# Performance work log

Measured on AMD Instinct MI355X. Metric: run time of the kernel, lower is better.

Reference implementation:

```python
import jax, jax.numpy as jnp
import numpy as np

T, B, D, H, L = 1024, 64, 512, 512, 2


def setup_inputs() -> dict:
    key = jax.random.key(0)
    ks = jax.random.split(key, 10)
    s = 1.0 / np.sqrt(D)
    return {
        "x": jax.random.normal(ks[0], (T, B, D), jnp.float32),
        "hidden": jax.random.normal(ks[1], (L, B, H), jnp.float32),
        "fc_w": jax.random.normal(ks[2], (D, D), jnp.float32) * s,
        "fc_b": jax.random.normal(ks[3], (D,), jnp.float32) * s,
        "w0": jax.random.normal(ks[4], (H, D), jnp.float32) * s,
        "b0": jax.random.normal(ks[5], (H,), jnp.float32) * s,
        "u0": jax.random.uniform(ks[6], (H,), jnp.float32, -1.0, 1.0),
        "w1": jax.random.normal(ks[7], (H, H), jnp.float32) * s,
        "b1": jax.random.normal(ks[8], (H,), jnp.float32) * s,
        "u1": jax.random.uniform(ks[9], (H,), jnp.float32, -1.0, 1.0),
    }


def _indrnn_layer(inp, h0, w, b, u):
    # Precompute input projection for all timesteps: [T, B, H]
    pre = jnp.einsum("tbd,hd->tbh", inp, w) + b

    def step(h, p):
        h_new = jax.nn.relu(p + u * h)  # elementwise recurrent weight
        return h_new, h_new

    h_last, outs = jax.lax.scan(step, h0, pre)
    return outs, h_last


def reference(x, hidden, fc_w, fc_b, w0, b0, u0, w1, b1, u1):
    # fc layer before the IndRNN stack
    x = jnp.einsum("tbd,ed->tbe", x, fc_w) + fc_b
    out0, h0 = _indrnn_layer(x, hidden[0], w0, b0, u0)
    out1, h1 = _indrnn_layer(out0, hidden[1], w1, b1, u1)
    hn = jnp.stack([h0, h1], axis=0)  # [L, B, H]
    return out1, hn
```

## Files before the change

kernel.cpp:

```cpp
#include <hip/hip_runtime.h>
#include <hip/hip_bf16.h>
#include <cstdint>
#include <cstddef>

#define T_DIM 1024
#define B_DIM 64
#define D_DIM 512
#define H_DIM 512
#define TBROWS (T_DIM * B_DIM)
#define BH (B_DIM * H_DIM)
#define TBH ((size_t)T_DIM * (size_t)BH)

typedef __bf16 bf16x8 __attribute__((ext_vector_type(8)));
typedef float floatx4 __attribute__((ext_vector_type(4)));

__device__ __forceinline__ void async_load16(const void* g, void* l) {
  __builtin_amdgcn_global_load_lds(
      (const __attribute__((address_space(1))) unsigned int*)g,
      (__attribute__((address_space(3))) unsigned int*)l,
      16, 0, 0);
}

__global__ __launch_bounds__(256) void cvt_bf16_kernel(
    const float* __restrict__ in, __bf16* __restrict__ out, long n) {
  long i = ((long)blockIdx.x * 256 + threadIdx.x) * 8;
  if (i + 8 <= n) {
    const float4 a = *(const float4*)(in + i);
    const float4 b = *(const float4*)(in + i + 4);
    bf16x8 v;
    v[0] = (__bf16)a.x; v[1] = (__bf16)a.y; v[2] = (__bf16)a.z; v[3] = (__bf16)a.w;
    v[4] = (__bf16)b.x; v[5] = (__bf16)b.y; v[6] = (__bf16)b.z; v[7] = (__bf16)b.w;
    *(bf16x8*)(out + i) = v;
  }
}

__global__ __launch_bounds__(256) void fuse_w_kernel(
    const float* __restrict__ w0, const float* __restrict__ fc_w,
    __bf16* __restrict__ W) {
  const int h = blockIdx.x >> 1;
  const int d = ((blockIdx.x & 1) << 8) + threadIdx.x;
  float a0 = 0.f, a1 = 0.f, a2 = 0.f, a3 = 0.f;
  for (int e = 0; e < D_DIM; e += 4) {
    a0 = fmaf(w0[h * D_DIM + e + 0], fc_w[(size_t)(e + 0) * D_DIM + d], a0);
    a1 = fmaf(w0[h * D_DIM + e + 1], fc_w[(size_t)(e + 1) * D_DIM + d], a1);
    a2 = fmaf(w0[h * D_DIM + e + 2], fc_w[(size_t)(e + 2) * D_DIM + d], a2);
    a3 = fmaf(w0[h * D_DIM + e + 3], fc_w[(size_t)(e + 3) * D_DIM + d], a3);
  }
  W[(size_t)h * D_DIM + d] = (__bf16)((a0 + a1) + (a2 + a3));
}

__global__ __launch_bounds__(256) void bcomb_kernel(
    const float* __restrict__ w0, const float* __restrict__ fc_b,
    const float* __restrict__ b0, float* __restrict__ bc) {
  const int h = blockIdx.x * 256 + threadIdx.x;
  float acc = b0[h];
  for (int e = 0; e < D_DIM; ++e)
    acc = fmaf(w0[(size_t)h * D_DIM + e], fc_b[e], acc);
  bc[h] = acc;
}

#define BM 128
#define BN 128
#define BK 32

__global__ __launch_bounds__(256) void gemm_bt_bias(
    const __bf16* __restrict__ A,
    const __bf16* __restrict__ Bm,
    const float* __restrict__ bias,
    float* __restrict__ C,
    int M, int N, int K) {
  __shared__ __bf16 As[BM * BK];
  __shared__ __bf16 Bs[BN * BK];

  const int tid = threadIdx.x;
  const int lane = tid & 63;
  const int wave = tid >> 6;
  const int nb = N / BN;
  const int bm = blockIdx.x / nb;
  const int bn = blockIdx.x % nb;
  const int m0 = bm * BM, n0 = bn * BN;

  floatx4 zero = {0.f, 0.f, 0.f, 0.f};
  floatx4 acc[4][4];
#pragma unroll
  for (int i = 0; i < 4; i++)
#pragma unroll
    for (int j = 0; j < 4; j++) acc[i][j] = zero;

  const int e0 = (wave * 2 + 0) * 64 + lane;
  const int e1 = (wave * 2 + 1) * 64 + lane;
  const int r0 = e0 >> 2, c0 = (e0 & 3) * 8;
  const int r1 = e1 >> 2, c1 = (e1 & 3) * 8;

  const int tm = (wave >> 1) * 64;
  const int tn = (wave & 1) * 64;
  const int lrow = lane & 15;
  const int lk = (lane >> 4) * 8;

  for (int k0 = 0; k0 < K; k0 += BK) {
    async_load16(&A[(size_t)(m0 + r0) * K + k0 + c0], &As[(wave * 2 + 0) * 512]);
    async_load16(&A[(size_t)(m0 + r1) * K + k0 + c1], &As[(wave * 2 + 1) * 512]);
    async_load16(&Bm[(size_t)(n0 + r0) * K + k0 + c0], &Bs[(wave * 2 + 0) * 512]);
    async_load16(&Bm[(size_t)(n0 + r1) * K + k0 + c1], &Bs[(wave * 2 + 1) * 512]);
    __syncthreads();

    bf16x8 af[4], bfr[4];
#pragma unroll
    for (int i = 0; i < 4; i++) {
      af[i]  = *(const bf16x8*)&As[(tm + i * 16 + lrow) * BK + lk];
      bfr[i] = *(const bf16x8*)&Bs[(tn + i * 16 + lrow) * BK + lk];
    }
#pragma unroll
    for (int i = 0; i < 4; i++)
#pragma unroll
      for (int j = 0; j < 4; j++)
        acc[i][j] = __builtin_amdgcn_mfma_f32_16x16x32_bf16(af[i], bfr[j],
                                                            acc[i][j], 0, 0, 0);
    __syncthreads();
  }

  const int ccol = lane & 15;
  const int crow = (lane >> 4) * 4;
  float bv[4];
#pragma unroll
  for (int j = 0; j < 4; j++) bv[j] = bias[n0 + tn + j * 16 + ccol];
#pragma unroll
  for (int i = 0; i < 4; i++) {
#pragma unroll
    for (int j = 0; j < 4; j++) {
      const size_t base =
          (size_t)(m0 + tm + i * 16 + crow) * N + (n0 + tn + j * 16 + ccol);
#pragma unroll
      for (int r = 0; r < 4; r++)
        C[base + (size_t)r * N] = acc[i][j][r] + bv[j];
    }
  }
}

template <bool BF16OUT>
__global__ __launch_bounds__(64) void scan_kernel(
    const float* __restrict__ pre,
    const float* __restrict__ h0,
    const float* __restrict__ u,
    void* __restrict__ outp,
    float* __restrict__ hn) {
  const int idx = blockIdx.x * 64 + threadIdx.x;
  const float uu = u[idx & (H_DIM - 1)];
  float h = h0[idx];
  __bf16* ob = (__bf16*)outp;
  float* of = (float*)outp;
  for (int t0 = 0; t0 < T_DIM; t0 += 32) {
    float v[32];
#pragma unroll
    for (int s = 0; s < 32; s++) v[s] = pre[(size_t)(t0 + s) * BH + idx];
#pragma unroll
    for (int s = 0; s < 32; s++) {
      h = fmaxf(fmaf(uu, h, v[s]), 0.0f);
      if (BF16OUT)
        ob[(size_t)(t0 + s) * BH + idx] = (__bf16)h;
      else
        of[(size_t)(t0 + s) * BH + idx] = h;
    }
  }
  hn[idx] = h;
}

extern "C" void kernel_launch(void* const* d_in, const int* in_sizes, int n_in,
                              void* d_out, int out_size, void* d_ws,
                              size_t ws_size, hipStream_t stream) {
  (void)in_sizes; (void)n_in; (void)out_size; (void)ws_size;
  const float* x      = (const float*)d_in[0];
  const float* hidden = (const float*)d_in[1];
  const float* fc_w   = (const float*)d_in[2];
  const float* fc_b   = (const float*)d_in[3];
  const float* w0     = (const float*)d_in[4];
  const float* b0     = (const float*)d_in[5];
  const float* u0     = (const float*)d_in[6];
  const float* w1     = (const float*)d_in[7];
  const float* b1     = (const float*)d_in[8];
  const float* u1     = (const float*)d_in[9];
  float* out = (float*)d_out;

  char* ws = (char*)d_ws;
  __bf16* xbf   = (__bf16*)ws;
  __bf16* Wc    = (__bf16*)(ws + TBH * 2);
  __bf16* w1bf  = (__bf16*)(ws + TBH * 2 + 512 * 1024);
  float*  bcomb = (float*)(ws + TBH * 2 + 1024 * 1024);

  float* pre = out;
  float* hn  = out + TBH;

  cvt_bf16_kernel<<<(int)(TBH / (256 * 8)), 256, 0, stream>>>(x, xbf, (long)TBH);
  cvt_bf16_kernel<<<(H_DIM * H_DIM) / (256 * 8), 256, 0, stream>>>(
      w1, w1bf, (long)(H_DIM * H_DIM));
  fuse_w_kernel<<<H_DIM * 2, 256, 0, stream>>>(w0, fc_w, Wc);
  bcomb_kernel<<<H_DIM / 256, 256, 0, stream>>>(w0, fc_b, b0, bcomb);
  gemm_bt_bias<<<(TBROWS / BM) * (H_DIM / BN), 256, 0, stream>>>(
      xbf, Wc, bcomb, pre, TBROWS, H_DIM, D_DIM);
  scan_kernel<true><<<BH / 64, 64, 0, stream>>>(pre, hidden, u0, (void*)xbf, hn);
  gemm_bt_bias<<<(TBROWS / BM) * (H_DIM / BN), 256, 0, stream>>>(
      xbf, w1bf, b1, pre, TBROWS, H_DIM, H_DIM);
  scan_kernel<false><<<BH / 64, 64, 0, stream>>>(pre, hidden + BH, u1,
                                                 (void*)pre, hn + BH);
}
```

Measured before the change: 491.9 us.

## Fuse fp32-to-bf16 conversion into GEMM, store preactivations in bf16, prefetch scan

The first GEMM now reads fp32 x directly into swizzled LDS and converts it to bf16 while building fragments, which removes the separate conversion pass over x. Both GEMMs write the preactivation tensor as bf16 into workspace rather than fp32, halving that intermediate's write and read traffic. The scan kernel double-buffers its loads so the next 32 timesteps are fetched while the current ones are computed. The trade-off is extra rounding of the preactivations to bf16, which may affect accuracy, and higher register pressure in the scan.

```diff
diff --git a/kernel.cpp b/kernel.cpp
--- a/kernel.cpp
+++ b/kernel.cpp
@@ -63,13 +63,13 @@
 #define BN 128
 #define BK 32
 
-__global__ __launch_bounds__(256) void gemm_bt_bias(
-    const __bf16* __restrict__ A,
+__global__ __launch_bounds__(256) void gemm_a32_bt_bias(
+    const float* __restrict__ A,
     const __bf16* __restrict__ Bm,
     const float* __restrict__ bias,
-    float* __restrict__ C,
+    __bf16* __restrict__ C,
     int M, int N, int K) {
-  __shared__ __bf16 As[BM * BK];
+  __shared__ float Asf[BM * BK];
   __shared__ __bf16 Bs[BN * BK];
 
   const int tid = threadIdx.x;
@@ -89,6 +89,99 @@
 
   const int e0 = (wave * 2 + 0) * 64 + lane;
   const int e1 = (wave * 2 + 1) * 64 + lane;
+  const int br0 = e0 >> 2, bc0 = (e0 & 3) * 8;
+  const int br1 = e1 >> 2, bc1 = (e1 & 3) * 8;
+
+  int ar[4], ac[4], abase[4];
+#pragma unroll
+  for (int j = 0; j < 4; j++) {
+    const int u = j * 256 + wave * 64 + lane;
+    ar[j] = u >> 3;
+    const int s = u & 7;
+    ac[j] = ((s - ar[j]) & 7) * 4;
+    abase[j] = (j * 256 + wave * 64) * 4;
+  }
+
+  const int tm = (wave >> 1) * 64;
+  const int tn = (wave & 1) * 64;
+  const int lrow = lane & 15;
+  const int lk = (lane >> 4) * 8;
+
+  for (int k0 = 0; k0 < K; k0 += BK) {
+#pragma unroll
+    for (int j = 0; j < 4; j++)
+      async_load16(&A[(size_t)(m0 + ar[j]) * K + k0 + ac[j]], &Asf[abase[j]]);
+    async_load16(&Bm[(size_t)(n0 + br0) * K + k0 + bc0], &Bs[(wave * 2 + 0) * 512]);
+    async_load16(&Bm[(size_t)(n0 + br1) * K + k0 + bc1], &Bs[(wave * 2 + 1) * 512]);
+    __syncthreads();
+
+    bf16x8 af[4], bfr[4];
+#pragma unroll
+    for (int i = 0; i < 4; i++) {
+      const int row = tm + i * 16 + lrow;
+      const int s0 = ((lk >> 2) + row) & 7;
+      const int s1 = ((lk >> 2) + 1 + row) & 7;
+      const float4 f0 = *(const float4*)&Asf[(row * 8 + s0) * 4];
+      const float4 f1 = *(const float4*)&Asf[(row * 8 + s1) * 4];
+      bf16x8 v;
+      v[0] = (__bf16)f0.x; v[1] = (__bf16)f0.y; v[2] = (__bf16)f0.z; v[3] = (__bf16)f0.w;
+      v[4] = (__bf16)f1.x; v[5] = (__bf16)f1.y; v[6] = (__bf16)f1.z; v[7] = (__bf16)f1.w;
+      af[i] = v;
+      bfr[i] = *(const bf16x8*)&Bs[(tn + i * 16 + lrow) * BK + lk];
+    }
+#pragma unroll
+    for (int i = 0; i < 4; i++)
+#pragma unroll
+      for (int j = 0; j < 4; j++)
+        acc[i][j] = __builtin_amdgcn_mfma_f32_16x16x32_bf16(af[i], bfr[j],
+                                                            acc[i][j], 0, 0, 0);
+    __syncthreads();
+  }
+
+  const int ccol = lane & 15;
+  const int crow = (lane >> 4) * 4;
+  float bv[4];
+#pragma unroll
+  for (int j = 0; j < 4; j++) bv[j] = bias[n0 + tn + j * 16 + ccol];
+#pragma unroll
+  for (int i = 0; i < 4; i++) {
+#pragma unroll
+    for (int j = 0; j < 4; j++) {
+      const size_t base =
+          (size_t)(m0 + tm + i * 16 + crow) * N + (n0 + tn + j * 16 + ccol);
+#pragma unroll
+      for (int r = 0; r < 4; r++)
+        C[base + (size_t)r * N] = (__bf16)(acc[i][j][r] + bv[j]);
+    }
+  }
+}
+
+__global__ __launch_bounds__(256) void gemm_bt_bias(
+    const __bf16* __restrict__ A,
+    const __bf16* __restrict__ Bm,
+    const float* __restrict__ bias,
+    __bf16* __restrict__ C,
+    int M, int N, int K) {
+  __shared__ __bf16 As[BM * BK];
+  __shared__ __bf16 Bs[BN * BK];
+
+  const int tid = threadIdx.x;
+  const int lane = tid & 63;
+  const int wave = tid >> 6;
+  const int nb = N / BN;
+  const int bm = blockIdx.x / nb;
+  const int bn = blockIdx.x % nb;
+  const int m0 = bm * BM, n0 = bn * BN;
+
+  floatx4 zero = {0.f, 0.f, 0.f, 0.f};
+  floatx4 acc[4][4];
+#pragma unroll
+  for (int i = 0; i < 4; i++)
+#pragma unroll
+    for (int j = 0; j < 4; j++) acc[i][j] = zero;
+
+  const int e0 = (wave * 2 + 0) * 64 + lane;
+  const int e1 = (wave * 2 + 1) * 64 + lane;
   const int r0 = e0 >> 2, c0 = (e0 & 3) * 8;
   const int r1 = e1 >> 2, c1 = (e1 & 3) * 8;
 
@@ -132,14 +225,14 @@
           (size_t)(m0 + tm + i * 16 + crow) * N + (n0 + tn + j * 16 + ccol);
 #pragma unroll
       for (int r = 0; r < 4; r++)
-        C[base + (size_t)r * N] = acc[i][j][r] + bv[j];
+        C[base + (size_t)r * N] = (__bf16)(acc[i][j][r] + bv[j]);
     }
   }
 }
 
 template <bool BF16OUT>
 __global__ __launch_bounds__(64) void scan_kernel(
-    const float* __restrict__ pre,
+    const __bf16* __restrict__ pre,
     const float* __restrict__ h0,
     const float* __restrict__ u,
     void* __restrict__ outp,
@@ -147,12 +240,21 @@
   const int idx = blockIdx.x * 64 + threadIdx.x;
   const float uu = u[idx & (H_DIM - 1)];
   float h = h0[idx];
-  __bf16* ob = (__bf16*)outp;
-  float* of = (float*)outp;
+  __bf16* __restrict__ ob = (__bf16*)outp;
+  float* __restrict__ of = (float*)outp;
+
+  float v[32];
+#pragma unroll
+  for (int s = 0; s < 32; s++) v[s] = (float)pre[(size_t)s * BH + idx];
+
   for (int t0 = 0; t0 < T_DIM; t0 += 32) {
-    float v[32];
-#pragma unroll
-    for (int s = 0; s < 32; s++) v[s] = pre[(size_t)(t0 + s) * BH + idx];
+    float w[32];
+    const bool more = (t0 + 32) < T_DIM;
+    if (more) {
+#pragma unroll
+      for (int s = 0; s < 32; s++)
+        w[s] = (float)pre[(size_t)(t0 + 32 + s) * BH + idx];
+    }
 #pragma unroll
     for (int s = 0; s < 32; s++) {
       h = fmaxf(fmaf(uu, h, v[s]), 0.0f);
@@ -160,6 +262,10 @@
         ob[(size_t)(t0 + s) * BH + idx] = (__bf16)h;
       else
         of[(size_t)(t0 + s) * BH + idx] = h;
+    }
+    if (more) {
+#pragma unroll
+      for (int s = 0; s < 32; s++) v[s] = w[s];
     }
   }
   hn[idx] = h;
@@ -182,24 +288,24 @@
   float* out = (float*)d_out;
 
   char* ws = (char*)d_ws;
-  __bf16* xbf   = (__bf16*)ws;
-  __bf16* Wc    = (__bf16*)(ws + TBH * 2);
-  __bf16* w1bf  = (__bf16*)(ws + TBH * 2 + 512 * 1024);
-  float*  bcomb = (float*)(ws + TBH * 2 + 1024 * 1024);
-
-  float* pre = out;
-  float* hn  = out + TBH;
-
-  cvt_bf16_kernel<<<(int)(TBH / (256 * 8)), 256, 0, stream>>>(x, xbf, (long)TBH);
+  __bf16* pre   = (__bf16*)ws;
+  __bf16* out0  = (__bf16*)(ws + TBH * 2);
+  char*   tail  = ws + 2 * TBH * 2;
+  __bf16* Wc    = (__bf16*)tail;
+  __bf16* w1bf  = (__bf16*)(tail + 512 * 1024);
+  float*  bcomb = (float*)(tail + 1024 * 1024);
+
+  float* hn = out + TBH;
+
   cvt_bf16_kernel<<<(H_DIM * H_DIM) / (256 * 8), 256, 0, stream>>>(
       w1, w1bf, (long)(H_DIM * H_DIM));
   fuse_w_kernel<<<H_DIM * 2, 256, 0, stream>>>(w0, fc_w, Wc);
   bcomb_kernel<<<H_DIM / 256, 256, 0, stream>>>(w0, fc_b, b0, bcomb);
+  gemm_a32_bt_bias<<<(TBROWS / BM) * (H_DIM / BN), 256, 0, stream>>>(
+      x, Wc, bcomb, pre, TBROWS, H_DIM, D_DIM);
+  scan_kernel<true><<<BH / 64, 64, 0, stream>>>(pre, hidden, u0, (void*)out0, hn);
   gemm_bt_bias<<<(TBROWS / BM) * (H_DIM / BN), 256, 0, stream>>>(
-      xbf, Wc, bcomb, pre, TBROWS, H_DIM, D_DIM);
-  scan_kernel<true><<<BH / 64, 64, 0, stream>>>(pre, hidden, u0, (void*)xbf, hn);
-  gemm_bt_bias<<<(TBROWS / BM) * (H_DIM / BN), 256, 0, stream>>>(
-      xbf, w1bf, b1, pre, TBROWS, H_DIM, H_DIM);
+      out0, w1bf, b1, pre, TBROWS, H_DIM, H_DIM);
   scan_kernel<false><<<BH / 64, 64, 0, stream>>>(pre, hidden + BH, u1,
-                                                 (void*)pre, hn + BH);
-}
+                                                 (void*)out, hn + BH);
+}
```

Result: faster. 468.1 us (-4.8%).

## Store GEMM pre-activations in bf16, prefetch scan inputs, merge prep kernels

Applied to the files above, without the earlier changes.

The GEMM epilogue now writes the pre-activation tensor as bf16 into workspace instead of fp32 into the output buffer, which halves the write traffic and the scan's read traffic. The scan kernel double-buffers 64 timesteps in registers so loads for the next chunk are issued while the current chunk is computed. The weight fusion, w1 conversion and bias combination are merged into one launch. Buffers are reorganised so layer-0 output has its own bf16 buffer. Rounding the pre-activations to bf16 adds precision loss, and the larger register arrays may reduce occupancy.

```diff
diff --git a/kernel.cpp b/kernel.cpp
--- a/kernel.cpp
+++ b/kernel.cpp
@@ -34,29 +34,38 @@
   }
 }
 
-__global__ __launch_bounds__(256) void fuse_w_kernel(
+__global__ __launch_bounds__(256) void prep_kernel(
     const float* __restrict__ w0, const float* __restrict__ fc_w,
-    __bf16* __restrict__ W) {
-  const int h = blockIdx.x >> 1;
-  const int d = ((blockIdx.x & 1) << 8) + threadIdx.x;
-  float a0 = 0.f, a1 = 0.f, a2 = 0.f, a3 = 0.f;
-  for (int e = 0; e < D_DIM; e += 4) {
-    a0 = fmaf(w0[h * D_DIM + e + 0], fc_w[(size_t)(e + 0) * D_DIM + d], a0);
-    a1 = fmaf(w0[h * D_DIM + e + 1], fc_w[(size_t)(e + 1) * D_DIM + d], a1);
-    a2 = fmaf(w0[h * D_DIM + e + 2], fc_w[(size_t)(e + 2) * D_DIM + d], a2);
-    a3 = fmaf(w0[h * D_DIM + e + 3], fc_w[(size_t)(e + 3) * D_DIM + d], a3);
-  }
-  W[(size_t)h * D_DIM + d] = (__bf16)((a0 + a1) + (a2 + a3));
-}
-
-__global__ __launch_bounds__(256) void bcomb_kernel(
-    const float* __restrict__ w0, const float* __restrict__ fc_b,
-    const float* __restrict__ b0, float* __restrict__ bc) {
-  const int h = blockIdx.x * 256 + threadIdx.x;
-  float acc = b0[h];
-  for (int e = 0; e < D_DIM; ++e)
-    acc = fmaf(w0[(size_t)h * D_DIM + e], fc_b[e], acc);
-  bc[h] = acc;
+    const float* __restrict__ fc_b, const float* __restrict__ b0,
+    const float* __restrict__ w1, __bf16* __restrict__ Wc,
+    __bf16* __restrict__ w1bf, float* __restrict__ bcomb) {
+  const int blk = blockIdx.x;
+  if (blk < 1024) {
+    const int h = blk >> 1;
+    const int d = ((blk & 1) << 8) + threadIdx.x;
+    float a0 = 0.f, a1 = 0.f, a2 = 0.f, a3 = 0.f;
+    for (int e = 0; e < D_DIM; e += 4) {
+      a0 = fmaf(w0[h * D_DIM + e + 0], fc_w[(size_t)(e + 0) * D_DIM + d], a0);
+      a1 = fmaf(w0[h * D_DIM + e + 1], fc_w[(size_t)(e + 1) * D_DIM + d], a1);
+      a2 = fmaf(w0[h * D_DIM + e + 2], fc_w[(size_t)(e + 2) * D_DIM + d], a2);
+      a3 = fmaf(w0[h * D_DIM + e + 3], fc_w[(size_t)(e + 3) * D_DIM + d], a3);
+    }
+    Wc[(size_t)h * D_DIM + d] = (__bf16)((a0 + a1) + (a2 + a3));
+  } else if (blk < 1152) {
+    const long i = ((long)(blk - 1024) * 256 + threadIdx.x) * 8;
+    const float4 a = *(const float4*)(w1 + i);
+    const float4 b = *(const float4*)(w1 + i + 4);
+    bf16x8 v;
+    v[0] = (__bf16)a.x; v[1] = (__bf16)a.y; v[2] = (__bf16)a.z; v[3] = (__bf16)a.w;
+    v[4] = (__bf16)b.x; v[5] = (__bf16)b.y; v[6] = (__bf16)b.z; v[7] = (__bf16)b.w;
+    *(bf16x8*)(w1bf + i) = v;
+  } else {
+    const int h = (blk - 1152) * 256 + threadIdx.x;
+    float acc = b0[h];
+    for (int e = 0; e < D_DIM; ++e)
+      acc = fmaf(w0[(size_t)h * D_DIM + e], fc_b[e], acc);
+    bcomb[h] = acc;
+  }
 }
 
 #define BM 128
@@ -67,7 +76,7 @@
     const __bf16* __restrict__ A,
     const __bf16* __restrict__ Bm,
     const float* __restrict__ bias,
-    float* __restrict__ C,
+    __bf16* __restrict__ C,
     int M, int N, int K) {
   __shared__ __bf16 As[BM * BK];
   __shared__ __bf16 Bs[BN * BK];
@@ -132,14 +141,14 @@
           (size_t)(m0 + tm + i * 16 + crow) * N + (n0 + tn + j * 16 + ccol);
 #pragma unroll
       for (int r = 0; r < 4; r++)
-        C[base + (size_t)r * N] = acc[i][j][r] + bv[j];
+        C[base + (size_t)r * N] = (__bf16)(acc[i][j][r] + bv[j]);
     }
   }
 }
 
 template <bool BF16OUT>
 __global__ __launch_bounds__(64) void scan_kernel(
-    const float* __restrict__ pre,
+    const __bf16* __restrict__ pre,
     const float* __restrict__ h0,
     const float* __restrict__ u,
     void* __restrict__ outp,
@@ -147,19 +156,32 @@
   const int idx = blockIdx.x * 64 + threadIdx.x;
   const float uu = u[idx & (H_DIM - 1)];
   float h = h0[idx];
-  __bf16* ob = (__bf16*)outp;
-  float* of = (float*)outp;
-  for (int t0 = 0; t0 < T_DIM; t0 += 32) {
-    float v[32];
-#pragma unroll
-    for (int s = 0; s < 32; s++) v[s] = pre[(size_t)(t0 + s) * BH + idx];
-#pragma unroll
-    for (int s = 0; s < 32; s++) {
+  __bf16* __restrict__ ob = (__bf16*)outp;
+  float* __restrict__ of = (float*)outp;
+
+  float v[64];
+#pragma unroll
+  for (int s = 0; s < 64; s++) v[s] = (float)pre[(size_t)s * BH + idx];
+
+  for (int t0 = 0; t0 < T_DIM; t0 += 64) {
+    float w[64];
+    const bool more = (t0 + 64) < T_DIM;
+    if (more) {
+#pragma unroll
+      for (int s = 0; s < 64; s++)
+        w[s] = (float)pre[(size_t)(t0 + 64 + s) * BH + idx];
+    }
+#pragma unroll
+    for (int s = 0; s < 64; s++) {
       h = fmaxf(fmaf(uu, h, v[s]), 0.0f);
       if (BF16OUT)
         ob[(size_t)(t0 + s) * BH + idx] = (__bf16)h;
       else
         of[(size_t)(t0 + s) * BH + idx] = h;
+    }
+    if (more) {
+#pragma unroll
+      for (int s = 0; s < 64; s++) v[s] = w[s];
     }
   }
   hn[idx] = h;
@@ -182,24 +204,23 @@
   float* out = (float*)d_out;
 
   char* ws = (char*)d_ws;
-  __bf16* xbf   = (__bf16*)ws;
-  __bf16* Wc    = (__bf16*)(ws + TBH * 2);
-  __bf16* w1bf  = (__bf16*)(ws + TBH * 2 + 512 * 1024);
-  float*  bcomb = (float*)(ws + TBH * 2 + 1024 * 1024);
-
-  float* pre = out;
-  float* hn  = out + TBH;
-
+  __bf16* xbf  = (__bf16*)ws;
+  __bf16* pre  = (__bf16*)(ws + TBH * 2);
+  __bf16* out0 = (__bf16*)(ws + 2 * TBH * 2);
+  char*   tail = ws + 3 * TBH * 2;
+  __bf16* Wc    = (__bf16*)tail;
+  __bf16* w1bf  = (__bf16*)(tail + 512 * 1024);
+  float*  bcomb = (float*)(tail + 1024 * 1024);
+
+  float* hn = out + TBH;
+
+  prep_kernel<<<1154, 256, 0, stream>>>(w0, fc_w, fc_b, b0, w1, Wc, w1bf, bcomb);
   cvt_bf16_kernel<<<(int)(TBH / (256 * 8)), 256, 0, stream>>>(x, xbf, (long)TBH);
-  cvt_bf16_kernel<<<(H_DIM * H_DIM) / (256 * 8), 256, 0, stream>>>(
-      w1, w1bf, (long)(H_DIM * H_DIM));
-  fuse_w_kernel<<<H_DIM * 2, 256, 0, stream>>>(w0, fc_w, Wc);
-  bcomb_kernel<<<H_DIM / 256, 256, 0, stream>>>(w0, fc_b, b0, bcomb);
   gemm_bt_bias<<<(TBROWS / BM) * (H_DIM / BN), 256, 0, stream>>>(
       xbf, Wc, bcomb, pre, TBROWS, H_DIM, D_DIM);
-  scan_kernel<true><<<BH / 64, 64, 0, stream>>>(pre, hidden, u0, (void*)xbf, hn);
+  scan_kernel<true><<<BH / 64, 64, 0, stream>>>(pre, hidden, u0, (void*)out0, hn);
   gemm_bt_bias<<<(TBROWS / BM) * (H_DIM / BN), 256, 0, stream>>>(
-      xbf, w1bf, b1, pre, TBROWS, H_DIM, H_DIM);
+      out0, w1bf, b1, pre, TBROWS, H_DIM, H_DIM);
   scan_kernel<false><<<BH / 64, 64, 0, stream>>>(pre, hidden + BH, u1,
-                                                 (void*)pre, hn + BH);
-}
+                                                 (void*)out, hn + BH);
+}
```

After: 500.8 us. About the same (+1.8%).
